# Kernel tuning notes

Measured on AMD Instinct MI355X. Metric: run time of the kernel, lower is better.

The kernel has to match this reference:

```python
import jax, jax.numpy as jnp
import numpy as np

N = 262144
D = 128      # input_dim
H = 64       # hidden size of each group head
G = 4        # num_groups
P = 4        # num_phases


def setup_inputs() -> dict:
    key = jax.random.key(0)
    k1, k2, k3, k4, k5, k6, k7 = jax.random.split(key, 7)
    h_int = jax.random.normal(k1, (N, D), dtype=jnp.float32)
    group_ids = jax.random.randint(k2, (N,), 0, G, dtype=jnp.int64)
    feasible_mask = jax.random.randint(k3, (N, P), 0, 2, dtype=jnp.int32).astype(jnp.bool_)
    # Stacked per-group head params: Linear(D->H), ReLU, Linear(H->P)
    W1 = jax.random.normal(k4, (G, D, H), dtype=jnp.float32) / np.sqrt(D)
    b1 = jax.random.normal(k5, (G, H), dtype=jnp.float32) * 0.01
    W2 = jax.random.normal(k6, (G, H, P), dtype=jnp.float32) / np.sqrt(H)
    b2 = jax.random.normal(k7, (G, P), dtype=jnp.float32) * 0.01
    return {"h_int": h_int, "group_ids": group_ids, "feasible_mask": feasible_mask,
            "W1": W1, "b1": b1, "W2": W2, "b2": b2}


def reference(h_int, group_ids, feasible_mask, W1, b1, W2, b2):
    # Dense grouped-GEMM: evaluate every head on every row, then select by group id.
    # hidden: [N, G, H]
    hidden = jax.nn.relu(jnp.einsum('nd,gdh->ngh', h_int, W1) + b1[None])
    # all_logits: [N, G, P]
    all_logits = jnp.einsum('ngh,ghp->ngp', hidden, W2) + b2[None]
    # select the row's own group head -> [N, P]
    gid = group_ids.astype(jnp.int32)[:, None, None]
    logits = jnp.take_along_axis(all_logits, gid, axis=1)[:, 0, :]
    logits = jnp.where(feasible_mask, logits, jnp.float32(-1e9))
    return jax.nn.softmax(logits, axis=-1)
```

## Files before the change

### kernel.cpp

```cpp
#include <hip/hip_runtime.h>
#include <hip/hip_bf16.h>
#include <cstdint>

#define NROWS 262144
#define DIM 128

typedef float f32x4 __attribute__((ext_vector_type(4)));
typedef short s16x8 __attribute__((ext_vector_type(8)));
typedef unsigned short u16x8 __attribute__((ext_vector_type(8)));
typedef unsigned int u32x4 __attribute__((ext_vector_type(4)));

__device__ __forceinline__ unsigned short cvbf(float f){
  unsigned u = __float_as_uint(f);
  return (unsigned short)((u + 0x8000u) >> 16);
}

__device__ __forceinline__ void ldsload16(const void* gp, void* lp){
  __builtin_amdgcn_global_load_lds((const __attribute__((address_space(1))) void*)gp,
                                   (__attribute__((address_space(3))) void*)lp,
                                   16, 0, 0);
}

__global__ void prep_kernel(const float* __restrict__ W1, const float* __restrict__ W2,
                            const void* __restrict__ gids_raw, const void* __restrict__ mask_raw,
                            unsigned char* __restrict__ ws){
  int tid = threadIdx.x, bid = blockIdx.x;
  if (bid < 16){
    int chunk = bid*256 + tid;
    int n    = chunk >> 4;
    int kb16 = chunk & 15;
    int d0   = kb16 * 8;
    int g = n >> 6, h = n & 63;
    u16x8 v;
#pragma unroll
    for (int j=0;j<8;++j) v[j] = cvbf(W1[((g*DIM) + d0 + j)*64 + h]);
    unsigned off = (unsigned)n*256 + (((unsigned)kb16*16) ^ (((unsigned)(n&7))<<4));
    *(u16x8*)(ws + off) = v;
  } else {
#pragma unroll
    for (int i=0;i<16;++i){
      int el = tid + i*256;
      int t  = el >> 6;
      int e  = el & 63;
      int g = t >> 4, p = t & 15;
      int h = (e & 32) | ((e & 4) << 2) | ((e >> 1) & 12) | (e & 3);
      float f = (p < 4) ? W2[(g*64 + h)*4 + p] : 0.0f;
      unsigned off = 65536u + (unsigned)t*128 + (((unsigned)(e*2)) ^ (((unsigned)(t&7))<<4));
      *(unsigned short*)(ws + off) = cvbf(f);
    }
    if (tid < 64){
      const int* g32 = (const int*)gids_raw;
      int accg = 0;
#pragma unroll
      for (int i=0;i<8;++i) accg |= g32[(tid*8 + i)*2 + 1];
      const unsigned char* m8 = (const unsigned char*)mask_raw;
      int accm = 0;
#pragma unroll
      for (int i=0;i<16;++i){
        int off = tid*16 + i;
        if (off & 3) accm |= m8[off];
      }
      unsigned long long bg = __ballot(accg != 0);
      unsigned long long bm = __ballot(accm != 0);
      if (tid == 0){
        *(int*)(ws + 73728) = (bg == 0ull) ? 1 : 0;
        *(int*)(ws + 73732) = (bm == 0ull) ? 2 : 0;
      }
    }
  }
}

#define LDS_W2T 65536
#define LDS_B1  (65536+8192)
#define LDS_TOTAL (65536+8192+1024)

__global__ __launch_bounds__(256, 2)
void actor_kernel(const float* __restrict__ X, const int* __restrict__ gids,
                  const unsigned char* __restrict__ fmask,
                  const float* __restrict__ b1, const float* __restrict__ b2,
                  const unsigned char* __restrict__ ws, float* __restrict__ out){
  __shared__ char smem[LDS_TOTAL];
  const int tid  = threadIdx.x;
  const int wave = tid >> 6, lane = tid & 63;
  const int q    = lane >> 4, rS = lane & 15;
  const int swzA = (rS & 7) << 4;

  const int gshift = *(const int*)(ws + 73728);
  const int mshift = *(const int*)(ws + 73732);

#pragma unroll
  for (int i=0;i<16;++i){
    int off = i*4096 + wave*1024;
    ldsload16(ws + off + lane*16, smem + off);
  }
#pragma unroll
  for (int i=0;i<2;++i){
    int off = i*4096 + wave*1024;
    ldsload16(ws + 65536 + off + lane*16, smem + LDS_W2T + off);
  }
  if (wave == 0)
    ldsload16((const unsigned char*)b1 + lane*16, smem + LDS_B1);
  __syncthreads();

  const long base = (long)blockIdx.x * 512 + wave * 128;
  const f32x4 z = (f32x4){0.f,0.f,0.f,0.f};

#pragma unroll 1
  for (int u=0; u<4; ++u){
    const long row0 = base + u*32 + rS;

    int gb0, gb1;
    u32x4 mb0, mb1;
    f32x4 xb[2][4][2];
    {
      gb0 = gids[(size_t)row0 << gshift];
      gb1 = gids[(size_t)(row0 + 16) << gshift];
      if (mshift){
        mb0 = *(const u32x4*)(fmask + row0*16);
        mb1 = *(const u32x4*)(fmask + (row0+16)*16);
      } else {
        unsigned w0 = *(const unsigned*)(fmask + row0*4);
        unsigned w1 = *(const unsigned*)(fmask + (row0+16)*4);
        mb0[0]=w0&0xffu; mb0[1]=(w0>>8)&0xffu; mb0[2]=(w0>>16)&0xffu; mb0[3]=w0>>24;
        mb1[0]=w1&0xffu; mb1[1]=(w1>>8)&0xffu; mb1[2]=(w1>>16)&0xffu; mb1[3]=w1>>24;
      }
      const float* xp0 = X + row0 * DIM + q*8;
      const float* xp1 = X + (row0 + 16) * DIM + q*8;
#pragma unroll
      for (int k=0;k<4;++k){
        xb[0][k][0] = *(const f32x4*)(xp0 + k*32);
        xb[0][k][1] = *(const f32x4*)(xp0 + k*32 + 4);
        xb[1][k][0] = *(const f32x4*)(xp1 + k*32);
        xb[1][k][1] = *(const f32x4*)(xp1 + k*32 + 4);
      }
    }
    __builtin_amdgcn_sched_barrier(0);

    s16x8 bfr[2][4];
#pragma unroll
    for (int nt=0;nt<2;++nt)
#pragma unroll
      for (int k=0;k<4;++k){
        s16x8 v;
#pragma unroll
        for (int j=0;j<4;++j){ v[j] = (short)cvbf(xb[nt][k][0][j]); v[j+4] = (short)cvbf(xb[nt][k][1][j]); }
        bfr[nt][k] = v;
      }
    __builtin_amdgcn_sched_barrier(0);

    f32x4 acc2[4][2];
#pragma unroll
    for (int p=0;p<8;++p){
      f32x4 aA0, aA1, aB0, aB1;
#pragma unroll
      for (int k=0;k<4;++k){
        const s16x8 sA = *(const s16x8*)(smem + ((2*p  )*16 + rS)*256 + ((k*64 + q*16) ^ swzA));
        const s16x8 sB = *(const s16x8*)(smem + ((2*p+1)*16 + rS)*256 + ((k*64 + q*16) ^ swzA));
        aA0 = __builtin_amdgcn_mfma_f32_16x16x32_bf16(sA, bfr[0][k], (k==0)? z : aA0, 0,0,0);
        aA1 = __builtin_amdgcn_mfma_f32_16x16x32_bf16(sA, bfr[1][k], (k==0)? z : aA1, 0,0,0);
        aB0 = __builtin_amdgcn_mfma_f32_16x16x32_bf16(sB, bfr[0][k], (k==0)? z : aB0, 0,0,0);
        aB1 = __builtin_amdgcn_mfma_f32_16x16x32_bf16(sB, bfr[1][k], (k==0)? z : aB1, 0,0,0);
      }
      const f32x4 b1A = *(const f32x4*)(smem + LDS_B1 + (2*p  )*64 + q*16);
      const f32x4 b1B = *(const f32x4*)(smem + LDS_B1 + (2*p+1)*64 + q*16);
      const s16x8 af = *(const s16x8*)(smem + LDS_W2T + ((p>>1)*16 + rS)*128
                                       + (((p&1)*64 + q*16) ^ swzA));
      {
        f32x4 vA = aA0 + b1A;
        f32x4 vB = aB0 + b1B;
#pragma unroll
        for (int j=0;j<4;++j){
          vA[j] = vA[j] > 0.f ? vA[j] : 0.f;
          vB[j] = vB[j] > 0.f ? vB[j] : 0.f;
        }
        s16x8 hf;
#pragma unroll
        for (int j=0;j<4;++j){ hf[j] = (short)cvbf(vA[j]); hf[j+4] = (short)cvbf(vB[j]); }
        acc2[p>>1][0] = __builtin_amdgcn_mfma_f32_16x16x32_bf16(
            af, hf, (p&1) ? acc2[p>>1][0] : z, 0,0,0);
      }
      {
        f32x4 vA = aA1 + b1A;
        f32x4 vB = aB1 + b1B;
#pragma unroll
        for (int j=0;j<4;++j){
          vA[j] = vA[j] > 0.f ? vA[j] : 0.f;
          vB[j] = vB[j] > 0.f ? vB[j] : 0.f;
        }
        s16x8 hf;
#pragma unroll
        for (int j=0;j<4;++j){ hf[j] = (short)cvbf(vA[j]); hf[j+4] = (short)cvbf(vB[j]); }
        acc2[p>>1][1] = __builtin_amdgcn_mfma_f32_16x16x32_bf16(
            af, hf, (p&1) ? acc2[p>>1][1] : z, 0,0,0);
      }
      __builtin_amdgcn_sched_barrier(0);
    }

    {
      int g = gb0;
      f32x4 lv = acc2[0][0];
      lv = (g==1) ? acc2[1][0] : lv;
      lv = (g==2) ? acc2[2][0] : lv;
      lv = (g==3) ? acc2[3][0] : lv;
      const f32x4 bs = *(const f32x4*)(b2 + g*4);
      f32x4 li;
#pragma unroll
      for (int p=0;p<4;++p)
        li[p] = mb0[p] ? (lv[p] + bs[p]) : -1e9f;
      float m = fmaxf(fmaxf(li[0],li[1]), fmaxf(li[2],li[3]));
      f32x4 e;
#pragma unroll
      for (int p=0;p<4;++p) e[p] = __expf(li[p] - m);
      float inv = 1.0f / (e[0]+e[1]+e[2]+e[3]);
      f32x4 o;
#pragma unroll
      for (int p=0;p<4;++p) o[p] = e[p] * inv;
      if (q == 0)
        *(f32x4*)(out + row0*4) = o;
    }
    {
      int g = gb1;
      f32x4 lv = acc2[0][1];
      lv = (g==1) ? acc2[1][1] : lv;
      lv = (g==2) ? acc2[2][1] : lv;
      lv = (g==3) ? acc2[3][1] : lv;
      const f32x4 bs = *(const f32x4*)(b2 + g*4);
      f32x4 li;
#pragma unroll
      for (int p=0;p<4;++p)
        li[p] = mb1[p] ? (lv[p] + bs[p]) : -1e9f;
      float m = fmaxf(fmaxf(li[0],li[1]), fmaxf(li[2],li[3]));
      f32x4 e;
#pragma unroll
      for (int p=0;p<4;++p) e[p] = __expf(li[p] - m);
      float inv = 1.0f / (e[0]+e[1]+e[2]+e[3]);
      f32x4 o;
#pragma unroll
      for (int p=0;p<4;++p) o[p] = e[p] * inv;
      if (q == 0)
        *(f32x4*)(out + (row0+16)*4) = o;
    }
  }
}

extern "C" void kernel_launch(void* const* d_in, const int* in_sizes, int n_in,
                              void* d_out, int out_size, void* d_ws, size_t ws_size,
                              hipStream_t stream){
  const float* X  = (const float*)d_in[0];
  const void*  gi = d_in[1];
  const void*  fm = d_in[2];
  const float* W1 = (const float*)d_in[3];
  const float* b1 = (const float*)d_in[4];
  const float* W2 = (const float*)d_in[5];
  const float* b2 = (const float*)d_in[6];
  unsigned char* ws = (unsigned char*)d_ws;
  float* out = (float*)d_out;

  prep_kernel<<<dim3(17), dim3(256), 0, stream>>>(W1, W2, gi, fm, ws);
  actor_kernel<<<dim3(512), dim3(256), 0, stream>>>(X, (const int*)gi,
                                                    (const unsigned char*)fm,
                                                    b1, b2, ws, out);
}
```

Measured before the change: 37.72 us.

## Sort rows by group and run only each row's own head

Adds a histogram, prefix-scan and scatter pass that bucket row indices by group id into 128-row padded segments. A new sorted actor kernel then loads a single group's weights per block and computes one head instead of all four, a quarter of the MFMA work. The price is three extra launches (one of them a single-block scan), gathered non-contiguous reads of X and the mask through the permutation, and scattered output writes. The old dense kernel is kept as a fallback when the workspace is too small.

```diff
diff --git a/kernel.cpp b/kernel.cpp
--- a/kernel.cpp
+++ b/kernel.cpp
@@ -4,6 +4,15 @@
 
 #define NROWS 262144
 #define DIM 128
+#define NMB  2052
+
+#define WS_GSHIFT 73728
+#define WS_MSHIFT 73732
+#define CNTB_OFF  73792
+#define SEGS_OFF  81984
+#define BSTART_OFF 82432
+#define PERM_OFF  90880
+#define WS_NEEDED (PERM_OFF + NMB*128*4)
 
 typedef float f32x4 __attribute__((ext_vector_type(4)));
 typedef short s16x8 __attribute__((ext_vector_type(8)));
@@ -63,10 +72,228 @@
       unsigned long long bg = __ballot(accg != 0);
       unsigned long long bm = __ballot(accm != 0);
       if (tid == 0){
-        *(int*)(ws + 73728) = (bg == 0ull) ? 1 : 0;
-        *(int*)(ws + 73732) = (bm == 0ull) ? 2 : 0;
-      }
-    }
+        *(int*)(ws + WS_GSHIFT) = (bg == 0ull) ? 1 : 0;
+        *(int*)(ws + WS_MSHIFT) = (bm == 0ull) ? 2 : 0;
+      }
+    }
+  }
+}
+
+__global__ void hist_kernel(const int* __restrict__ gids, unsigned char* __restrict__ ws){
+  __shared__ int h[4];
+  int tid = threadIdx.x, bid = blockIdx.x;
+  if (tid < 4) h[tid] = 0;
+  __syncthreads();
+  const int gshift = *(const int*)(ws + WS_GSHIFT);
+#pragma unroll
+  for (int i=0;i<2;++i){
+    int row = bid*512 + tid + i*256;
+    int g = gids[(size_t)row << gshift] & 3;
+    atomicAdd(&h[g], 1);
+  }
+  __syncthreads();
+  if (tid < 4) ((int*)(ws + CNTB_OFF))[bid*4 + tid] = h[tid];
+}
+
+__global__ void seg_kernel(unsigned char* __restrict__ ws){
+  __shared__ int A[4][512], B[4][512];
+  __shared__ int segL[5], totL[4];
+  int tid = threadIdx.x;
+  const int* cntb = (const int*)(ws + CNTB_OFF);
+  for (int e = tid; e < 2048; e += 256){
+    int g = e >> 9, i = e & 511;
+    A[g][i] = cntb[i*4 + g];
+  }
+  __syncthreads();
+  bool ab = true;
+  for (int off = 1; off < 512; off <<= 1){
+    for (int e = tid; e < 2048; e += 256){
+      int g = e >> 9, i = e & 511;
+      int v = ab ? A[g][i] : B[g][i];
+      if (i >= off) v += ab ? A[g][i-off] : B[g][i-off];
+      if (ab) B[g][i] = v; else A[g][i] = v;
+    }
+    __syncthreads();
+    ab = !ab;
+  }
+  if (tid == 0){
+    int s = 0;
+    for (int g=0; g<4; ++g){
+      int tot = ab ? A[g][511] : B[g][511];
+      totL[g] = tot;
+      segL[g] = s;
+      s += ((tot + 127) >> 7) << 7;
+    }
+    segL[4] = s;
+    int* segs = (int*)(ws + SEGS_OFF);
+    for (int g=0; g<5; ++g) segs[g] = segL[g];
+  }
+  __syncthreads();
+  int* bstart = (int*)(ws + BSTART_OFF);
+  for (int e = tid; e < 2048; e += 256){
+    int g = e >> 9, i = e & 511;
+    int incl = ab ? A[g][i] : B[g][i];
+    bstart[i*4 + g] = segL[g] + incl - cntb[i*4 + g];
+  }
+  int* perm = (int*)(ws + PERM_OFF);
+  for (int g=0; g<4; ++g){
+    int beg = segL[g] + totL[g];
+    int end = (g < 3) ? segL[g+1] : segL[4];
+    for (int i = beg + tid; i < end; i += 256) perm[i] = -1;
+  }
+  for (int i = segL[4] + tid; i < NMB*128; i += 256) perm[i] = -1;
+}
+
+__global__ void scat_kernel(const int* __restrict__ gids, unsigned char* __restrict__ ws){
+  __shared__ int cur[4];
+  int tid = threadIdx.x, bid = blockIdx.x;
+  const int gshift = *(const int*)(ws + WS_GSHIFT);
+  if (tid < 4) cur[tid] = ((const int*)(ws + BSTART_OFF))[bid*4 + tid];
+  __syncthreads();
+  int* perm = (int*)(ws + PERM_OFF);
+#pragma unroll
+  for (int i=0;i<2;++i){
+    int row = bid*512 + tid + i*256;
+    int g = gids[(size_t)row << gshift] & 3;
+    int pos = atomicAdd(&cur[g], 1);
+    perm[pos] = row;
+  }
+}
+
+#define W2G_OFF 16384
+#define B1G_OFF (16384+2048)
+#define LDS_S_TOTAL (16384+2048+256)
+
+__global__ __launch_bounds__(256, 2)
+void actor_sorted(const float* __restrict__ X,
+                  const unsigned char* __restrict__ fmask,
+                  const float* __restrict__ b1, const float* __restrict__ b2,
+                  const unsigned char* __restrict__ ws, float* __restrict__ out){
+  __shared__ char smem[LDS_S_TOTAL];
+  const int tid  = threadIdx.x;
+  const int wave = tid >> 6, lane = tid & 63;
+  const int q    = lane >> 4, rS = lane & 15;
+  const int swzA = (rS & 7) << 4;
+
+  const int mshift = *(const int*)(ws + WS_MSHIFT);
+  const int* segs = (const int*)(ws + SEGS_OFF);
+  const int p0 = blockIdx.x * 128;
+  const int g = (p0 >= segs[1]) + (p0 >= segs[2]) + (p0 >= segs[3]);
+
+#pragma unroll
+  for (int i=0;i<4;++i){
+    int off = i*4096 + wave*1024;
+    ldsload16(ws + g*16384 + off + lane*16, smem + off);
+  }
+  if (wave < 2)
+    ldsload16(ws + 65536 + g*2048 + wave*1024 + lane*16, smem + W2G_OFF + wave*1024 + lane*16);
+  if (wave == 2 && lane < 16)
+    ldsload16((const unsigned char*)b1 + g*256 + lane*16, smem + B1G_OFF + lane*16);
+  __syncthreads();
+
+  const f32x4 z = (f32x4){0.f,0.f,0.f,0.f};
+  const int pos = p0 + wave*32;
+  const int* perm = (const int*)(ws + PERM_OFF);
+  const int r0 = perm[pos + rS];
+  const int r1 = perm[pos + 16 + rS];
+  const int v0 = (r0 >= 0), v1 = (r1 >= 0);
+  const long rr0 = v0 ? r0 : 0, rr1 = v1 ? r1 : 0;
+
+  u32x4 mb0, mb1;
+  if (mshift){
+    mb0 = *(const u32x4*)(fmask + rr0*16);
+    mb1 = *(const u32x4*)(fmask + rr1*16);
+  } else {
+    unsigned w0 = *(const unsigned*)(fmask + rr0*4);
+    unsigned w1 = *(const unsigned*)(fmask + rr1*4);
+    mb0[0]=w0&0xffu; mb0[1]=(w0>>8)&0xffu; mb0[2]=(w0>>16)&0xffu; mb0[3]=w0>>24;
+    mb1[0]=w1&0xffu; mb1[1]=(w1>>8)&0xffu; mb1[2]=(w1>>16)&0xffu; mb1[3]=w1>>24;
+  }
+
+  f32x4 xb[2][4][2];
+  {
+    const float* xp0 = X + rr0 * DIM + q*8;
+    const float* xp1 = X + rr1 * DIM + q*8;
+#pragma unroll
+    for (int k=0;k<4;++k){
+      xb[0][k][0] = *(const f32x4*)(xp0 + k*32);
+      xb[0][k][1] = *(const f32x4*)(xp0 + k*32 + 4);
+      xb[1][k][0] = *(const f32x4*)(xp1 + k*32);
+      xb[1][k][1] = *(const f32x4*)(xp1 + k*32 + 4);
+    }
+  }
+  __builtin_amdgcn_sched_barrier(0);
+
+  s16x8 bfr[2][4];
+#pragma unroll
+  for (int nt=0;nt<2;++nt)
+#pragma unroll
+    for (int k=0;k<4;++k){
+      s16x8 v;
+#pragma unroll
+      for (int j=0;j<4;++j){ v[j] = (short)cvbf(xb[nt][k][0][j]); v[j+4] = (short)cvbf(xb[nt][k][1][j]); }
+      bfr[nt][k] = v;
+    }
+  __builtin_amdgcn_sched_barrier(0);
+
+  f32x4 acc2[2];
+#pragma unroll
+  for (int p=0;p<2;++p){
+    f32x4 aA0, aA1, aB0, aB1;
+#pragma unroll
+    for (int k=0;k<4;++k){
+      const s16x8 sA = *(const s16x8*)(smem + ((2*p  )*16 + rS)*256 + ((k*64 + q*16) ^ swzA));
+      const s16x8 sB = *(const s16x8*)(smem + ((2*p+1)*16 + rS)*256 + ((k*64 + q*16) ^ swzA));
+      aA0 = __builtin_amdgcn_mfma_f32_16x16x32_bf16(sA, bfr[0][k], (k==0)? z : aA0, 0,0,0);
+      aA1 = __builtin_amdgcn_mfma_f32_16x16x32_bf16(sA, bfr[1][k], (k==0)? z : aA1, 0,0,0);
+      aB0 = __builtin_amdgcn_mfma_f32_16x16x32_bf16(sB, bfr[0][k], (k==0)? z : aB0, 0,0,0);
+      aB1 = __builtin_amdgcn_mfma_f32_16x16x32_bf16(sB, bfr[1][k], (k==0)? z : aB1, 0,0,0);
+    }
+    const f32x4 b1A = *(const f32x4*)(smem + B1G_OFF + (2*p  )*64 + q*16);
+    const f32x4 b1B = *(const f32x4*)(smem + B1G_OFF + (2*p+1)*64 + q*16);
+    const s16x8 af = *(const s16x8*)(smem + W2G_OFF + rS*128 + ((p*64 + q*16) ^ swzA));
+    {
+      f32x4 vA = aA0 + b1A, vB = aB0 + b1B;
+#pragma unroll
+      for (int j=0;j<4;++j){ vA[j] = vA[j] > 0.f ? vA[j] : 0.f; vB[j] = vB[j] > 0.f ? vB[j] : 0.f; }
+      s16x8 hf;
+#pragma unroll
+      for (int j=0;j<4;++j){ hf[j] = (short)cvbf(vA[j]); hf[j+4] = (short)cvbf(vB[j]); }
+      acc2[0] = __builtin_amdgcn_mfma_f32_16x16x32_bf16(af, hf, p ? acc2[0] : z, 0,0,0);
+    }
+    {
+      f32x4 vA = aA1 + b1A, vB = aB1 + b1B;
+#pragma unroll
+      for (int j=0;j<4;++j){ vA[j] = vA[j] > 0.f ? vA[j] : 0.f; vB[j] = vB[j] > 0.f ? vB[j] : 0.f; }
+      s16x8 hf;
+#pragma unroll
+      for (int j=0;j<4;++j){ hf[j] = (short)cvbf(vA[j]); hf[j+4] = (short)cvbf(vB[j]); }
+      acc2[1] = __builtin_amdgcn_mfma_f32_16x16x32_bf16(af, hf, p ? acc2[1] : z, 0,0,0);
+    }
+    __builtin_amdgcn_sched_barrier(0);
+  }
+
+  const f32x4 bs = *(const f32x4*)(b2 + g*4);
+#pragma unroll
+  for (int nt=0;nt<2;++nt){
+    u32x4 mb = nt ? mb1 : mb0;
+    f32x4 lv = acc2[nt];
+    f32x4 li;
+#pragma unroll
+    for (int p=0;p<4;++p)
+      li[p] = mb[p] ? (lv[p] + bs[p]) : -1e9f;
+    float m = fmaxf(fmaxf(li[0],li[1]), fmaxf(li[2],li[3]));
+    f32x4 e;
+#pragma unroll
+    for (int p=0;p<4;++p) e[p] = __expf(li[p] - m);
+    float inv = 1.0f / (e[0]+e[1]+e[2]+e[3]);
+    f32x4 o;
+#pragma unroll
+    for (int p=0;p<4;++p) o[p] = e[p] * inv;
+    int valid = nt ? v1 : v0;
+    long r = nt ? rr1 : rr0;
+    if (q == 0 && valid)
+      *(f32x4*)(out + r*4) = o;
   }
 }
 
@@ -75,18 +302,18 @@
 #define LDS_TOTAL (65536+8192+1024)
 
 __global__ __launch_bounds__(256, 2)
-void actor_kernel(const float* __restrict__ X, const int* __restrict__ gids,
-                  const unsigned char* __restrict__ fmask,
-                  const float* __restrict__ b1, const float* __restrict__ b2,
-                  const unsigned char* __restrict__ ws, float* __restrict__ out){
+void actor_dense(const float* __restrict__ X, const int* __restrict__ gids,
+                 const unsigned char* __restrict__ fmask,
+                 const float* __restrict__ b1, const float* __restrict__ b2,
+                 const unsigned char* __restrict__ ws, float* __restrict__ out){
   __shared__ char smem[LDS_TOTAL];
   const int tid  = threadIdx.x;
   const int wave = tid >> 6, lane = tid & 63;
   const int q    = lane >> 4, rS = lane & 15;
   const int swzA = (rS & 7) << 4;
 
-  const int gshift = *(const int*)(ws + 73728);
-  const int mshift = *(const int*)(ws + 73732);
+  const int gshift = *(const int*)(ws + WS_GSHIFT);
+  const int mshift = *(const int*)(ws + WS_MSHIFT);
 
 #pragma unroll
   for (int i=0;i<16;++i){
@@ -108,7 +335,6 @@
 #pragma unroll 1
   for (int u=0; u<4; ++u){
     const long row0 = base + u*32 + rS;
-
     int gb0, gb1;
     u32x4 mb0, mb1;
     f32x4 xb[2][4][2];
@@ -166,47 +392,39 @@
       const s16x8 af = *(const s16x8*)(smem + LDS_W2T + ((p>>1)*16 + rS)*128
                                        + (((p&1)*64 + q*16) ^ swzA));
       {
-        f32x4 vA = aA0 + b1A;
-        f32x4 vB = aB0 + b1B;
-#pragma unroll
-        for (int j=0;j<4;++j){
-          vA[j] = vA[j] > 0.f ? vA[j] : 0.f;
-          vB[j] = vB[j] > 0.f ? vB[j] : 0.f;
-        }
+        f32x4 vA = aA0 + b1A, vB = aB0 + b1B;
+#pragma unroll
+        for (int j=0;j<4;++j){ vA[j] = vA[j] > 0.f ? vA[j] : 0.f; vB[j] = vB[j] > 0.f ? vB[j] : 0.f; }
         s16x8 hf;
 #pragma unroll
         for (int j=0;j<4;++j){ hf[j] = (short)cvbf(vA[j]); hf[j+4] = (short)cvbf(vB[j]); }
-        acc2[p>>1][0] = __builtin_amdgcn_mfma_f32_16x16x32_bf16(
-            af, hf, (p&1) ? acc2[p>>1][0] : z, 0,0,0);
+        acc2[p>>1][0] = __builtin_amdgcn_mfma_f32_16x16x32_bf16(af, hf, (p&1) ? acc2[p>>1][0] : z, 0,0,0);
       }
       {
-        f32x4 vA = aA1 + b1A;
-        f32x4 vB = aB1 + b1B;
-#pragma unroll
-        for (int j=0;j<4;++j){
-          vA[j] = vA[j] > 0.f ? vA[j] : 0.f;
-          vB[j] = vB[j] > 0.f ? vB[j] : 0.f;
-        }
+        f32x4 vA = aA1 + b1A, vB = aB1 + b1B;
+#pragma unroll
+        for (int j=0;j<4;++j){ vA[j] = vA[j] > 0.f ? vA[j] : 0.f; vB[j] = vB[j] > 0.f ? vB[j] : 0.f; }
         s16x8 hf;
 #pragma unroll
         for (int j=0;j<4;++j){ hf[j] = (short)cvbf(vA[j]); hf[j+4] = (short)cvbf(vB[j]); }
-        acc2[p>>1][1] = __builtin_amdgcn_mfma_f32_16x16x32_bf16(
-            af, hf, (p&1) ? acc2[p>>1][1] : z, 0,0,0);
+        acc2[p>>1][1] = __builtin_amdgcn_mfma_f32_16x16x32_bf16(af, hf, (p&1) ? acc2[p>>1][1] : z, 0,0,0);
       }
       __builtin_amdgcn_sched_barrier(0);
     }
 
-    {
-      int g = gb0;
-      f32x4 lv = acc2[0][0];
-      lv = (g==1) ? acc2[1][0] : lv;
-      lv = (g==2) ? acc2[2][0] : lv;
-      lv = (g==3) ? acc2[3][0] : lv;
+#pragma unroll
+    for (int nt=0;nt<2;++nt){
+      int g = nt ? gb1 : gb0;
+      u32x4 mb = nt ? mb1 : mb0;
+      f32x4 lv = acc2[0][nt];
+      lv = (g==1) ? acc2[1][nt] : lv;
+      lv = (g==2) ? acc2[2][nt] : lv;
+      lv = (g==3) ? acc2[3][nt] : lv;
       const f32x4 bs = *(const f32x4*)(b2 + g*4);
       f32x4 li;
 #pragma unroll
       for (int p=0;p<4;++p)
-        li[p] = mb0[p] ? (lv[p] + bs[p]) : -1e9f;
+        li[p] = mb[p] ? (lv[p] + bs[p]) : -1e9f;
       float m = fmaxf(fmaxf(li[0],li[1]), fmaxf(li[2],li[3]));
       f32x4 e;
 #pragma unroll
@@ -216,29 +434,7 @@
 #pragma unroll
       for (int p=0;p<4;++p) o[p] = e[p] * inv;
       if (q == 0)
-        *(f32x4*)(out + row0*4) = o;
-    }
-    {
-      int g = gb1;
-      f32x4 lv = acc2[0][1];
-      lv = (g==1) ? acc2[1][1] : lv;
-      lv = (g==2) ? acc2[2][1] : lv;
-      lv = (g==3) ? acc2[3][1] : lv;
-      const f32x4 bs = *(const f32x4*)(b2 + g*4);
-      f32x4 li;
-#pragma unroll
-      for (int p=0;p<4;++p)
-        li[p] = mb1[p] ? (lv[p] + bs[p]) : -1e9f;
-      float m = fmaxf(fmaxf(li[0],li[1]), fmaxf(li[2],li[3]));
-      f32x4 e;
-#pragma unroll
-      for (int p=0;p<4;++p) e[p] = __expf(li[p] - m);
-      float inv = 1.0f / (e[0]+e[1]+e[2]+e[3]);
-      f32x4 o;
-#pragma unroll
-      for (int p=0;p<4;++p) o[p] = e[p] * inv;
-      if (q == 0)
-        *(f32x4*)(out + (row0+16)*4) = o;
+        *(f32x4*)(out + (row0 + nt*16)*4) = o;
     }
   }
 }
@@ -257,7 +453,16 @@
   float* out = (float*)d_out;
 
   prep_kernel<<<dim3(17), dim3(256), 0, stream>>>(W1, W2, gi, fm, ws);
-  actor_kernel<<<dim3(512), dim3(256), 0, stream>>>(X, (const int*)gi,
-                                                    (const unsigned char*)fm,
-                                                    b1, b2, ws, out);
-}
+
+  if (ws_size >= (size_t)WS_NEEDED){
+    hist_kernel<<<dim3(512), dim3(256), 0, stream>>>((const int*)gi, ws);
+    seg_kernel <<<dim3(1),   dim3(256), 0, stream>>>(ws);
+    scat_kernel<<<dim3(512), dim3(256), 0, stream>>>((const int*)gi, ws);
+    actor_sorted<<<dim3(NMB), dim3(256), 0, stream>>>(X, (const unsigned char*)fm,
+                                                      b1, b2, ws, out);
+  } else {
+    actor_dense<<<dim3(512), dim3(256), 0, stream>>>(X, (const int*)gi,
+                                                     (const unsigned char*)fm,
+                                                     b1, b2, ws, out);
+  }
+}
```

Result: slower. 52.93 us (+40.3%).
